# Performance work log

Hardware: AMD Instinct MI355X
Metric: run time of the kernel (lower is better)

The kernel has to match this reference:

```python
import jax, jax.numpy as jnp
import numpy as np

D_MODEL = 1024
N_HEADS = 16
HEAD_DIM = D_MODEL // N_HEADS
ROPE_THETA = 10000.0


def _apply_rope(t, pos):
    # t: [B, H, S, hd]; pos: [B, S] int. Half-split (NeoX-style) rotation.
    hd = t.shape[-1]
    inv_freq = 1.0 / (ROPE_THETA ** (jnp.arange(0, hd, 2, dtype=t.dtype) / hd))  # [hd/2]
    ang = pos.astype(t.dtype)[:, None, :, None] * inv_freq  # [B, 1, S, hd/2]
    cos, sin = jnp.cos(ang), jnp.sin(ang)
    t1, t2 = t[..., 0::2], t[..., 1::2]
    r1 = t1 * cos - t2 * sin
    r2 = t1 * sin + t2 * cos
    # interleave back
    return jnp.stack([r1, r2], axis=-1).reshape(t.shape)


def setup_inputs() -> dict:
    key = jax.random.key(0)
    k1, k2, k3 = jax.random.split(key, 3)
    B, S = 4, 2048
    x = jax.random.normal(k1, (B, S, D_MODEL), dtype=jnp.float32)
    positions = jnp.broadcast_to(jnp.arange(S, dtype=jnp.int32), (B, S))
    Wqkv = jax.random.normal(k2, (3 * D_MODEL, D_MODEL), dtype=jnp.float32) * (1.0 / np.sqrt(D_MODEL))
    bqkv = jnp.zeros((3 * D_MODEL,), dtype=jnp.float32)
    Wo = jax.random.normal(k3, (D_MODEL, D_MODEL), dtype=jnp.float32) * (1.0 / np.sqrt(D_MODEL))
    bo = jnp.zeros((D_MODEL,), dtype=jnp.float32)
    return {"x": x, "positions": positions, "Wqkv": Wqkv, "bqkv": bqkv, "Wo": Wo, "bo": bo}


def reference(x, positions, Wqkv, bqkv, Wo, bo):
    B, S, D = x.shape
    # fused QKV projection (torch Linear: x @ W^T + b)
    qkv = x @ Wqkv.T + bqkv                      # [B, S, 3D]
    q, k, v = jnp.split(qkv, 3, axis=-1)
    def to_heads(t):
        return t.reshape(B, S, N_HEADS, HEAD_DIM).transpose(0, 2, 1, 3)  # [B, H, S, hd]
    q, k, v = to_heads(q), to_heads(k), to_heads(v)
    q = _apply_rope(q, positions)
    k = _apply_rope(k, positions)
    scale = 1.0 / np.sqrt(HEAD_DIM)
    scores = jnp.einsum('bhqd,bhkd->bhqk', q, k) * scale   # [B, H, S, S]
    causal = jnp.tril(jnp.ones((S, S), dtype=bool))
    scores = jnp.where(causal, scores, jnp.finfo(scores.dtype).min)
    attn = jax.nn.softmax(scores, axis=-1)
    h = jnp.einsum('bhqk,bhkd->bhqd', attn, v)             # [B, H, S, hd]
    h = h.transpose(0, 2, 1, 3).reshape(B, S, D)
    return h @ Wo.T + bo
```

## Files before the change

### kernel.cpp

```cpp
#include <hip/hip_runtime.h>

#define DEV static __device__ __forceinline__

typedef __attribute__((ext_vector_type(8))) short short8;
typedef __attribute__((ext_vector_type(4))) short short4v;
typedef __attribute__((ext_vector_type(4))) float f32x4;
typedef __attribute__((ext_vector_type(4))) unsigned short ushort4v;
typedef __attribute__((ext_vector_type(4))) float float4v;

#define DM 1024
#define NH 16
#define HD 64
#define SS 2048
#define TOK 8192

DEV unsigned short f2bf(float f) {
  union { float f; unsigned u; } v; v.f = f;
  unsigned r = v.u + 0x7FFFu + ((v.u >> 16) & 1u);
  return (unsigned short)(r >> 16);
}
DEV float bf2f(unsigned short h) {
  union { unsigned u; float f; } v; v.u = ((unsigned)h) << 16;
  return v.f;
}

#define MFMA16x32(a, b, c) __builtin_amdgcn_mfma_f32_16x16x32_bf16((a), (b), (c), 0, 0, 0)

DEV f32x4 mfma_pv(short4v a, short4v b, f32x4 c) {
#if __has_builtin(__builtin_amdgcn_mfma_f32_16x16x16bf16_1k)
  return __builtin_amdgcn_mfma_f32_16x16x16bf16_1k(a, b, c, 0, 0, 0);
#else
  f32x4 d;
  asm("v_mfma_f32_16x16x16_bf16 %0, %1, %2, %3" : "=&v"(d) : "v"(a), "v"(b), "v"(c));
  return d;
#endif
}

DEV void gload_lds16(const unsigned short* g, unsigned short* l) {
  __builtin_amdgcn_global_load_lds(
      (const __attribute__((address_space(1))) void*)g,
      (__attribute__((address_space(3))) void*)l, 16, 0, 0);
}

__global__ __launch_bounds__(256) void k_cvt(const float* __restrict__ in,
                                             unsigned short* __restrict__ out, int n4) {
  int i = blockIdx.x * 256 + threadIdx.x;
  if (i >= n4) return;
  float4v v = ((const float4v*)in)[i];
  ushort4v o;
  o[0] = f2bf(v[0]); o[1] = f2bf(v[1]); o[2] = f2bf(v[2]); o[3] = f2bf(v[3]);
  ((ushort4v*)out)[i] = o;
}

__global__ __launch_bounds__(256) void k_tab(const int* __restrict__ pos,
                                             float* __restrict__ tc, float* __restrict__ ts) {
  int i = blockIdx.x * 256 + threadIdx.x;
  int t = i >> 5, fi = i & 31;
  float p = (float)pos[t];
  float inv = powf(10000.0f, -(float)fi / 32.0f);
  float a = p * inv;
  float sv, cv;
  sincosf(a, &sv, &cv);
  tc[i] = cv;
  ts[i] = sv;
}

template <int MODE>
__global__ __launch_bounds__(512) void k_gemm3(
    const unsigned short* __restrict__ A, const unsigned short* __restrict__ Bm,
    const float* __restrict__ bias, void* __restrict__ out0, void* __restrict__ out1,
    void* __restrict__ out2, const float* __restrict__ tabc,
    const float* __restrict__ tabs, int M, int N, int K) {
  __shared__ __align__(16) unsigned short Abuf[3][256 * 64];
  __shared__ __align__(16) unsigned short Bbuf[3][128 * 64];
  const int tid = threadIdx.x;
  const int wid = tid >> 6, lane = tid & 63;
  const int l16 = lane & 15, lq = lane >> 4;
  const int wr = wid >> 1, wc = wid & 1;
  const int r8 = lane >> 3, c8 = lane & 7;
  const int NT = K >> 6;
  const int sx = l16 & 7;

  const int gx = N >> 7;
  const int nwg = gx * (M >> 8);
  const int chunk = nwg >> 3;
  const int bid = blockIdx.x;
  const int virt = (bid & 7) * chunk + (bid >> 3);
  const int m0 = (virt / gx) << 8;
  const int n0 = (virt % gx) << 7;

#define STAGE_G3(T, BSEL)                                                           \
  {                                                                                 \
    int k0_ = (T) << 6;                                                             \
    unsigned short* ab_ = Abuf[BSEL];                                               \
    unsigned short* bb_ = Bbuf[BSEL];                                               \
    _Pragma("unroll")                                                               \
    for (int i_ = 0; i_ < 4; ++i_) {                                                \
      int c_ = wid * 4 + i_;                                                        \
      gload_lds16(A + (size_t)(m0 + c_ * 8 + r8) * K + k0_ + ((c8 ^ r8) << 3),      \
                  &ab_[c_ * 512]);                                                  \
    }                                                                               \
    _Pragma("unroll")                                                               \
    for (int i_ = 0; i_ < 2; ++i_) {                                                \
      int c_ = wid * 2 + i_;                                                        \
      gload_lds16(Bm + (size_t)(n0 + c_ * 8 + r8) * K + k0_ + ((c8 ^ r8) << 3),     \
                  &bb_[c_ * 512]);                                                  \
    }                                                                               \
  }

  f32x4 acc[4][4];
#pragma unroll
  for (int i = 0; i < 4; i++)
#pragma unroll
    for (int j = 0; j < 4; j++) acc[i][j] = (f32x4){0.f, 0.f, 0.f, 0.f};

  STAGE_G3(0, 0)
  STAGE_G3(1, 1)
  asm volatile("s_waitcnt vmcnt(6)" ::: "memory");
  __builtin_amdgcn_s_barrier();
  __builtin_amdgcn_sched_barrier(0);

  int cb = 0, sb = 2;
  for (int t = 0; t < NT; ++t) {
    if (t + 2 < NT) STAGE_G3(t + 2, sb)
    const unsigned short* Ab = Abuf[cb];
    const unsigned short* Bb = Bbuf[cb];
#pragma unroll
    for (int kk = 0; kk < 2; ++kk) {
      int sw0 = ((kk * 4 + lq) ^ sx) << 3;
      short8 af[4], bfr[4];
#pragma unroll
      for (int mi = 0; mi < 4; ++mi)
        af[mi] = *(const short8*)&Ab[(wr * 64 + mi * 16 + l16) * 64 + sw0];
#pragma unroll
      for (int ni = 0; ni < 4; ++ni)
        bfr[ni] = *(const short8*)&Bb[(wc * 64 + ni * 16 + l16) * 64 + sw0];
#pragma unroll
      for (int mi = 0; mi < 4; ++mi)
#pragma unroll
        for (int ni = 0; ni < 4; ++ni)
          acc[mi][ni] = MFMA16x32(af[mi], bfr[ni], acc[mi][ni]);
    }
    if (t + 1 < NT) {
      if (t + 3 <= NT) {
        asm volatile("s_waitcnt vmcnt(6)" ::: "memory");
      } else {
        asm volatile("s_waitcnt vmcnt(0)" ::: "memory");
      }
      __builtin_amdgcn_s_barrier();
      __builtin_amdgcn_sched_barrier(0);
    }
    cb = (cb == 2) ? 0 : cb + 1;
    sb = (sb == 2) ? 0 : sb + 1;
  }
#undef STAGE_G3

  if (MODE == 0) {
    float* C = (float*)out0;
#pragma unroll
    for (int mi = 0; mi < 4; ++mi) {
      int row = m0 + wr * 64 + mi * 16 + lq * 4;
#pragma unroll
      for (int ni = 0; ni < 4; ++ni) {
        int col = n0 + wc * 64 + ni * 16 + l16;
        float bv = bias[col];
#pragma unroll
        for (int j = 0; j < 4; ++j)
          C[(size_t)(row + j) * N + col] = acc[mi][ni][j] + bv;
      }
    }
  } else {
    unsigned short* Qb = (unsigned short*)out0;
    unsigned short* Kb = (unsigned short*)out1;
    unsigned short* Vt = (unsigned short*)out2;
    int sel0 = n0 >> 10;
#pragma unroll
    for (int mi = 0; mi < 4; ++mi) {
      int row = m0 + wr * 64 + mi * 16 + lq * 4;
#pragma unroll
      for (int ni = 0; ni < 4; ++ni) {
        int col = n0 + wc * 64 + ni * 16 + l16;
        int hh = (col >> 6) & 15;
        int d = col & 63;
        float bv = bias[col];
        if (sel0 < 2) {
          unsigned short* P = sel0 ? Kb : Qb;
          int pfr = d >> 1;
          size_t p = ((size_t)((row >> 11) * NH + hh) * SS + (row & 2047)) * 64 + d;
#pragma unroll
          for (int j = 0; j < 4; ++j) {
            float val = acc[mi][ni][j] + bv;
            float part = __shfl_xor(val, 1, 64);
            int rr = row + j;
            float cv = tabc[((size_t)rr << 5) + pfr];
            float sv = tabs[((size_t)rr << 5) + pfr];
            float outv = (d & 1) ? (part * sv + val * cv)
                                 : (val * cv - part * sv);
            P[p + (size_t)j * 64] = f2bf(outv);
          }
        } else {
          size_t p = ((size_t)((row >> 11) * NH + hh) * 64 + d) * SS + (row & 2047);
          ushort4v o;
#pragma unroll
          for (int j = 0; j < 4; ++j) o[j] = f2bf(acc[mi][ni][j] + bv);
          *(ushort4v*)&Vt[p] = o;
        }
      }
    }
  }
}

__global__ __launch_bounds__(512) void k_attn(const unsigned short* __restrict__ Q,
                                              const unsigned short* __restrict__ K,
                                              const unsigned short* __restrict__ Vt,
                                              unsigned short* __restrict__ H) {
  __shared__ __align__(16) unsigned short Kbuf[2 * 4096];
  __shared__ __align__(16) unsigned short Vbuf[2 * 4096];

  int lin = blockIdx.x;
  int bh = lin & 63;
  int g = 15 - (lin >> 6);
  int b = bh >> 4, h = bh & 15;
  int tid = threadIdx.x;
  int wid = tid >> 6, lane = tid & 63;
  int l16 = lane & 15, lq = lane >> 4;
  int sx = l16 & 7;
  const unsigned short* Qh = Q + (size_t)bh * SS * 64;
  const unsigned short* Kh = K + (size_t)bh * SS * 64;
  const unsigned short* Vh = Vt + (size_t)bh * 64 * SS;

  int qbase = g * 128 + wid * 16;
  int qrow = qbase + l16;
  int ktmax = (qbase + 15) >> 6;
  int ntk = 2 * g + 2;

  short8 aq[2];
  {
    const unsigned short* qp = Qh + (size_t)qrow * 64 + lq * 8;
    aq[0] = *(const short8*)qp;
    aq[1] = *(const short8*)(qp + 32);
  }
  f32x4 o[4];
#pragma unroll
  for (int i = 0; i < 4; ++i) o[i] = (f32x4){0.f, 0.f, 0.f, 0.f};
  float lsum = 0.f;

  {
    int c = tid;
    int row = c >> 3, col = ((c & 7) ^ (row & 7)) << 3;
    gload_lds16(Kh + (size_t)row * 64 + col, &Kbuf[c * 8]);
    gload_lds16(Vh + (size_t)row * SS + col, &Vbuf[c * 8]);
  }
  __syncthreads();

  int cur = 0;
  for (int kt = 0; kt < ntk; ++kt) {
    if (kt + 1 < ntk) {
      int kb1 = (kt + 1) << 6;
      int nb_ = (cur ^ 1) * 4096;
      int c = tid;
      int row = c >> 3, col = ((c & 7) ^ (row & 7)) << 3;
      gload_lds16(Kh + (size_t)(kb1 + row) * 64 + col, &Kbuf[nb_ + c * 8]);
      gload_lds16(Vh + (size_t)row * SS + kb1 + col, &Vbuf[nb_ + c * 8]);
    }
    if (kt <= ktmax) {
      int kb = kt << 6;
      const unsigned short* Kb_ = &Kbuf[cur * 4096];
      const unsigned short* Vb_ = &Vbuf[cur * 4096];

      f32x4 sacc[4];
#pragma unroll
      for (int nb = 0; nb < 4; ++nb) {
        int r = nb * 16 + l16;
        short8 bk0 = *(const short8*)&Kb_[r * 64 + ((lq ^ sx) << 3)];
        short8 bk1 = *(const short8*)&Kb_[r * 64 + (((4 | lq) ^ sx) << 3)];
        f32x4 z = (f32x4){0.f, 0.f, 0.f, 0.f};
        z = MFMA16x32(bk0, aq[0], z);
        z = MFMA16x32(bk1, aq[1], z);
        sacc[nb] = z;
      }
      float sc[4][4];
#pragma unroll
      for (int nb = 0; nb < 4; ++nb)
#pragma unroll
        for (int j = 0; j < 4; ++j) sc[nb][j] = sacc[nb][j] * 0.18033688f;
      if (kt == ktmax) {
#pragma unroll
        for (int nb = 0; nb < 4; ++nb)
#pragma unroll
          for (int j = 0; j < 4; ++j) {
            int key = kb + nb * 16 + lq * 4 + j;
            if (key > qrow) sc[nb][j] = -1e30f;
          }
      }
      short4v pa[4];
#pragma unroll
      for (int nb = 0; nb < 4; ++nb) {
        float pv[4];
#pragma unroll
        for (int j = 0; j < 4; ++j) {
          float e;
          asm("v_exp_f32 %0, %1" : "=v"(e) : "v"(sc[nb][j]));
          lsum += e;
          pv[j] = e;
        }
        union { unsigned u[2]; short4v s4; } pk;
        asm("v_cvt_pk_bf16_f32 %0, %1, %2" : "=v"(pk.u[0]) : "v"(pv[0]), "v"(pv[1]));
        asm("v_cvt_pk_bf16_f32 %0, %1, %2" : "=v"(pk.u[1]) : "v"(pv[2]), "v"(pv[3]));
        pa[nb] = pk.s4;
      }
#pragma unroll
      for (int ni = 0; ni < 4; ++ni) {
        int row = ni * 16 + l16;
        f32x4 acc = o[ni];
#pragma unroll
        for (int nb = 0; nb < 4; ++nb) {
          int ch = (2 * nb + (lq >> 1)) ^ sx;
          short4v bv = *(const short4v*)&Vb_[row * 64 + ch * 8 + ((lq & 1) << 2)];
          acc = mfma_pv(pa[nb], bv, acc);
        }
        o[ni] = acc;
      }
    }
    __syncthreads();
    cur ^= 1;
  }

  float red = lsum;
  red += __shfl_xor(red, 16, 64);
  red += __shfl_xor(red, 32, 64);
  float inv[4];
#pragma unroll
  for (int j = 0; j < 4; ++j) {
    int src = (lane & 48) + ((lane >> 4) & 3) * 4 + j;
    inv[j] = 1.0f / __shfl(red, src, 64);
  }
#pragma unroll
  for (int ni = 0; ni < 4; ++ni) {
    int d = h * 64 + ni * 16 + l16;
#pragma unroll
    for (int j = 0; j < 4; ++j) {
      int s = qbase + lq * 4 + j;
      H[((size_t)(b * SS + s)) * 1024 + d] = f2bf(o[ni][j] * inv[j]);
    }
  }
}

extern "C" void kernel_launch(void* const* d_in, const int* in_sizes, int n_in,
                              void* d_out, int out_size, void* d_ws, size_t ws_size,
                              hipStream_t stream) {
  const float* x    = (const float*)d_in[0];
  const int*   pos  = (const int*)d_in[1];
  const float* Wqkv = (const float*)d_in[2];
  const float* bqkv = (const float*)d_in[3];
  const float* Wo   = (const float*)d_in[4];
  const float* bo   = (const float*)d_in[5];
  float* out = (float*)d_out;

  char* w = (char*)d_ws;
  unsigned short* x_bf    = (unsigned short*)(w + 0);
  unsigned short* h_bf    = x_bf;
  unsigned short* wqkv_bf = (unsigned short*)(w + 16777216);
  unsigned short* wo_bf   = (unsigned short*)(w + 23068672);
  unsigned short* Qb      = (unsigned short*)(w + 25165824);
  unsigned short* Kb      = (unsigned short*)(w + 41943040);
  unsigned short* Vt      = (unsigned short*)(w + 58720256);
  float* tabc             = (float*)(w + 75497472);
  float* tabs             = (float*)(w + 76546048);

  k_cvt<<<8192, 256, 0, stream>>>(x, x_bf, 2097152);
  k_cvt<<<3072, 256, 0, stream>>>(Wqkv, wqkv_bf, 786432);
  k_cvt<<<1024, 256, 0, stream>>>(Wo, wo_bf, 262144);
  k_tab<<<1024, 256, 0, stream>>>(pos, tabc, tabs);
  k_gemm3<1><<<768, 512, 0, stream>>>(x_bf, wqkv_bf, bqkv, Qb, Kb, Vt, tabc, tabs, TOK, 3072, DM);
  k_attn<<<1024, 512, 0, stream>>>(Qb, Kb, Vt, h_bf);
  k_gemm3<0><<<256, 512, 0, stream>>>(h_bf, wo_bf, bo, out, nullptr, nullptr, tabc, tabs, TOK, DM, DM);
}
```

Baseline: 186.7 us.

## Double query rows per attention wave, merge prep kernels, use 2D GEMM grid

The attention kernel now gives each wave two 16-row query fragments (256 queries per block), so each K/V tile loaded into LDS is reused by twice as many rows and the block count is halved. The weight conversions and the RoPE table kernel are merged into one launch to cut launch overhead. The GEMMs drop the XCD-aware swizzled block mapping in favour of a plain 2D grid. Risks: higher register pressure in attention under the (512,4) launch bound, fewer blocks for load balance across the causal triangle, and worse L2 locality from losing the swizzle.

```diff
diff --git a/kernel.cpp b/kernel.cpp
--- a/kernel.cpp
+++ b/kernel.cpp
@@ -52,17 +52,37 @@
   ((ushort4v*)out)[i] = o;
 }
 
-__global__ __launch_bounds__(256) void k_tab(const int* __restrict__ pos,
-                                             float* __restrict__ tc, float* __restrict__ ts) {
-  int i = blockIdx.x * 256 + threadIdx.x;
-  int t = i >> 5, fi = i & 31;
-  float p = (float)pos[t];
-  float inv = powf(10000.0f, -(float)fi / 32.0f);
-  float a = p * inv;
-  float sv, cv;
-  sincosf(a, &sv, &cv);
-  tc[i] = cv;
-  ts[i] = sv;
+__global__ __launch_bounds__(256) void k_prep(const float* __restrict__ Wqkv,
+                                              unsigned short* __restrict__ wqkv_bf,
+                                              const float* __restrict__ Wo,
+                                              unsigned short* __restrict__ wo_bf,
+                                              const int* __restrict__ pos,
+                                              float* __restrict__ tc,
+                                              float* __restrict__ ts) {
+  int blk = blockIdx.x;
+  if (blk < 3072) {
+    int i = blk * 256 + threadIdx.x;
+    float4v v = ((const float4v*)Wqkv)[i];
+    ushort4v o;
+    o[0] = f2bf(v[0]); o[1] = f2bf(v[1]); o[2] = f2bf(v[2]); o[3] = f2bf(v[3]);
+    ((ushort4v*)wqkv_bf)[i] = o;
+  } else if (blk < 4096) {
+    int i = (blk - 3072) * 256 + threadIdx.x;
+    float4v v = ((const float4v*)Wo)[i];
+    ushort4v o;
+    o[0] = f2bf(v[0]); o[1] = f2bf(v[1]); o[2] = f2bf(v[2]); o[3] = f2bf(v[3]);
+    ((ushort4v*)wo_bf)[i] = o;
+  } else {
+    int i = (blk - 4096) * 256 + threadIdx.x;
+    int t = i >> 5, fi = i & 31;
+    float p = (float)pos[t];
+    float inv = powf(10000.0f, -(float)fi / 32.0f);
+    float a = p * inv;
+    float sv, cv;
+    sincosf(a, &sv, &cv);
+    tc[i] = cv;
+    ts[i] = sv;
+  }
 }
 
 template <int MODE>
@@ -81,13 +101,8 @@
   const int NT = K >> 6;
   const int sx = l16 & 7;
 
-  const int gx = N >> 7;
-  const int nwg = gx * (M >> 8);
-  const int chunk = nwg >> 3;
-  const int bid = blockIdx.x;
-  const int virt = (bid & 7) * chunk + (bid >> 3);
-  const int m0 = (virt / gx) << 8;
-  const int n0 = (virt % gx) << 7;
+  const int m0 = blockIdx.y << 8;
+  const int n0 = blockIdx.x << 7;
 
 #define STAGE_G3(T, BSEL)                                                           \
   {                                                                                 \
@@ -210,16 +225,16 @@
   }
 }
 
-__global__ __launch_bounds__(512) void k_attn(const unsigned short* __restrict__ Q,
-                                              const unsigned short* __restrict__ K,
-                                              const unsigned short* __restrict__ Vt,
-                                              unsigned short* __restrict__ H) {
+__global__ __launch_bounds__(512, 4) void k_attn(const unsigned short* __restrict__ Q,
+                                                 const unsigned short* __restrict__ K,
+                                                 const unsigned short* __restrict__ Vt,
+                                                 unsigned short* __restrict__ H) {
   __shared__ __align__(16) unsigned short Kbuf[2 * 4096];
   __shared__ __align__(16) unsigned short Vbuf[2 * 4096];
 
   int lin = blockIdx.x;
   int bh = lin & 63;
-  int g = 15 - (lin >> 6);
+  int g = 7 - (lin >> 6);
   int b = bh >> 4, h = bh & 15;
   int tid = threadIdx.x;
   int wid = tid >> 6, lane = tid & 63;
@@ -229,21 +244,25 @@
   const unsigned short* Kh = K + (size_t)bh * SS * 64;
   const unsigned short* Vh = Vt + (size_t)bh * 64 * SS;
 
-  int qbase = g * 128 + wid * 16;
-  int qrow = qbase + l16;
-  int ktmax = (qbase + 15) >> 6;
-  int ntk = 2 * g + 2;
-
-  short8 aq[2];
-  {
-    const unsigned short* qp = Qh + (size_t)qrow * 64 + lq * 8;
-    aq[0] = *(const short8*)qp;
-    aq[1] = *(const short8*)(qp + 32);
-  }
-  f32x4 o[4];
-#pragma unroll
-  for (int i = 0; i < 4; ++i) o[i] = (f32x4){0.f, 0.f, 0.f, 0.f};
-  float lsum = 0.f;
+  int qbase = g * 256 + wid * 32;
+  int ktmax = (qbase + 31) >> 6;
+  int ntk = 4 * g + 4;
+
+  short8 aq[2][2];
+#pragma unroll
+  for (int rf = 0; rf < 2; ++rf) {
+    const unsigned short* qp = Qh + (size_t)(qbase + rf * 16 + l16) * 64 + lq * 8;
+    aq[rf][0] = *(const short8*)qp;
+    aq[rf][1] = *(const short8*)(qp + 32);
+  }
+  f32x4 o[2][4];
+  float lsum[2];
+#pragma unroll
+  for (int rf = 0; rf < 2; ++rf) {
+    lsum[rf] = 0.f;
+#pragma unroll
+    for (int i = 0; i < 4; ++i) o[rf][i] = (f32x4){0.f, 0.f, 0.f, 0.f};
+  }
 
   {
     int c = tid;
@@ -268,80 +287,85 @@
       const unsigned short* Kb_ = &Kbuf[cur * 4096];
       const unsigned short* Vb_ = &Vbuf[cur * 4096];
 
-      f32x4 sacc[4];
+      f32x4 sacc[2][4];
 #pragma unroll
       for (int nb = 0; nb < 4; ++nb) {
         int r = nb * 16 + l16;
         short8 bk0 = *(const short8*)&Kb_[r * 64 + ((lq ^ sx) << 3)];
         short8 bk1 = *(const short8*)&Kb_[r * 64 + (((4 | lq) ^ sx) << 3)];
-        f32x4 z = (f32x4){0.f, 0.f, 0.f, 0.f};
-        z = MFMA16x32(bk0, aq[0], z);
-        z = MFMA16x32(bk1, aq[1], z);
-        sacc[nb] = z;
-      }
-      float sc[4][4];
-#pragma unroll
-      for (int nb = 0; nb < 4; ++nb)
-#pragma unroll
-        for (int j = 0; j < 4; ++j) sc[nb][j] = sacc[nb][j] * 0.18033688f;
-      if (kt == ktmax) {
-#pragma unroll
-        for (int nb = 0; nb < 4; ++nb)
+        f32x4 z0 = (f32x4){0.f, 0.f, 0.f, 0.f};
+        z0 = MFMA16x32(bk0, aq[0][0], z0);
+        z0 = MFMA16x32(bk1, aq[0][1], z0);
+        sacc[0][nb] = z0;
+        f32x4 z1 = (f32x4){0.f, 0.f, 0.f, 0.f};
+        z1 = MFMA16x32(bk0, aq[1][0], z1);
+        z1 = MFMA16x32(bk1, aq[1][1], z1);
+        sacc[1][nb] = z1;
+      }
+      bool diag = (kt == ktmax);
+      short4v pa[2][4];
+#pragma unroll
+      for (int rf = 0; rf < 2; ++rf) {
+        int qrow = qbase + rf * 16 + l16;
+#pragma unroll
+        for (int nb = 0; nb < 4; ++nb) {
+          float pv[4];
 #pragma unroll
           for (int j = 0; j < 4; ++j) {
-            int key = kb + nb * 16 + lq * 4 + j;
-            if (key > qrow) sc[nb][j] = -1e30f;
+            float s = sacc[rf][nb][j] * 0.18033688f;
+            if (diag) {
+              int key = kb + nb * 16 + lq * 4 + j;
+              if (key > qrow) s = -1e30f;
+            }
+            float e;
+            asm("v_exp_f32 %0, %1" : "=v"(e) : "v"(s));
+            lsum[rf] += e;
+            pv[j] = e;
           }
-      }
-      short4v pa[4];
-#pragma unroll
-      for (int nb = 0; nb < 4; ++nb) {
-        float pv[4];
-#pragma unroll
-        for (int j = 0; j < 4; ++j) {
-          float e;
-          asm("v_exp_f32 %0, %1" : "=v"(e) : "v"(sc[nb][j]));
-          lsum += e;
-          pv[j] = e;
+          union { unsigned u[2]; short4v s4; } pk;
+          asm("v_cvt_pk_bf16_f32 %0, %1, %2" : "=v"(pk.u[0]) : "v"(pv[0]), "v"(pv[1]));
+          asm("v_cvt_pk_bf16_f32 %0, %1, %2" : "=v"(pk.u[1]) : "v"(pv[2]), "v"(pv[3]));
+          pa[rf][nb] = pk.s4;
         }
-        union { unsigned u[2]; short4v s4; } pk;
-        asm("v_cvt_pk_bf16_f32 %0, %1, %2" : "=v"(pk.u[0]) : "v"(pv[0]), "v"(pv[1]));
-        asm("v_cvt_pk_bf16_f32 %0, %1, %2" : "=v"(pk.u[1]) : "v"(pv[2]), "v"(pv[3]));
-        pa[nb] = pk.s4;
       }
 #pragma unroll
       for (int ni = 0; ni < 4; ++ni) {
         int row = ni * 16 + l16;
-        f32x4 acc = o[ni];
+        f32x4 a0 = o[0][ni], a1 = o[1][ni];
 #pragma unroll
         for (int nb = 0; nb < 4; ++nb) {
           int ch = (2 * nb + (lq >> 1)) ^ sx;
           short4v bv = *(const short4v*)&Vb_[row * 64 + ch * 8 + ((lq & 1) << 2)];
-          acc = mfma_pv(pa[nb], bv, acc);
+          a0 = mfma_pv(pa[0][nb], bv, a0);
+          a1 = mfma_pv(pa[1][nb], bv, a1);
         }
-        o[ni] = acc;
+        o[0][ni] = a0;
+        o[1][ni] = a1;
       }
     }
     __syncthreads();
     cur ^= 1;
   }
 
-  float red = lsum;
-  red += __shfl_xor(red, 16, 64);
-  red += __shfl_xor(red, 32, 64);
-  float inv[4];
-#pragma unroll
-  for (int j = 0; j < 4; ++j) {
-    int src = (lane & 48) + ((lane >> 4) & 3) * 4 + j;
-    inv[j] = 1.0f / __shfl(red, src, 64);
-  }
-#pragma unroll
-  for (int ni = 0; ni < 4; ++ni) {
-    int d = h * 64 + ni * 16 + l16;
+#pragma unroll
+  for (int rf = 0; rf < 2; ++rf) {
+    float red = lsum[rf];
+    red += __shfl_xor(red, 16, 64);
+    red += __shfl_xor(red, 32, 64);
+    float inv[4];
 #pragma unroll
     for (int j = 0; j < 4; ++j) {
-      int s = qbase + lq * 4 + j;
-      H[((size_t)(b * SS + s)) * 1024 + d] = f2bf(o[ni][j] * inv[j]);
+      int src = (lane & 48) + ((lane >> 4) & 3) * 4 + j;
+      inv[j] = 1.0f / __shfl(red, src, 64);
+    }
+#pragma unroll
+    for (int ni = 0; ni < 4; ++ni) {
+      int d = h * 64 + ni * 16 + l16;
+#pragma unroll
+      for (int j = 0; j < 4; ++j) {
+        int s = qbase + rf * 16 + lq * 4 + j;
+        H[((size_t)(b * SS + s)) * 1024 + d] = f2bf(o[rf][ni][j] * inv[j]);
+      }
     }
   }
 }
@@ -369,10 +393,8 @@
   float* tabs             = (float*)(w + 76546048);
 
   k_cvt<<<8192, 256, 0, stream>>>(x, x_bf, 2097152);
-  k_cvt<<<3072, 256, 0, stream>>>(Wqkv, wqkv_bf, 786432);
-  k_cvt<<<1024, 256, 0, stream>>>(Wo, wo_bf, 262144);
-  k_tab<<<1024, 256, 0, stream>>>(pos, tabc, tabs);
-  k_gemm3<1><<<768, 512, 0, stream>>>(x_bf, wqkv_bf, bqkv, Qb, Kb, Vt, tabc, tabs, TOK, 3072, DM);
-  k_attn<<<1024, 512, 0, stream>>>(Qb, Kb, Vt, h_bf);
-  k_gemm3<0><<<256, 512, 0, stream>>>(h_bf, wo_bf, bo, out, nullptr, nullptr, tabc, tabs, TOK, DM, DM);
-}
+  k_prep<<<5120, 256, 0, stream>>>(Wqkv, wqkv_bf, Wo, wo_bf, pos, tabc, tabs);
+  k_gemm3<1><<<dim3(24, 32), 512, 0, stream>>>(x_bf, wqkv_bf, bqkv, Qb, Kb, Vt, tabc, tabs, TOK, 3072, DM);
+  k_attn<<<512, 512, 0, stream>>>(Qb, Kb, Vt, h_bf);
+  k_gemm3<0><<<dim3(8, 32), 512, 0, stream>>>(h_bf, wo_bf, bo, out, nullptr, nullptr, tabc, tabs, TOK, DM, DM);
+}
```

Measured after the change: 201.7 us. 8.0% more time.
